# Performance work log

Measured on AMD Instinct MI355X. Metric: run time of the kernel, lower is better.

Reference implementation:

```python
import jax, jax.numpy as jnp
import numpy as np


def kmax_dmp(x, pool_ranges, k_per, K):
    """Vectorized dynamic k-max pooling (order-preserving top-k along time).

    x: [B, T, C] float. pool_ranges: [B] int (per-sample valid prefix length).
    k_per: [B] int (per-sample k, k_per[i] <= pool_ranges[i]). K: static max k.
    Returns [B, K, C]; rows beyond k_per[i] are zero-padded (like pad_sequence).
    """
    B, T, C = x.shape
    neg = jnp.finfo(x.dtype).min
    valid = jnp.arange(T)[None, :] < pool_ranges[:, None]            # [B,T]
    xm = jnp.where(valid[:, :, None], x, neg)
    vals, idx = jax.lax.top_k(jnp.swapaxes(xm, 1, 2), K)             # [B,C,K]
    keep = jnp.arange(K)[None, None, :] < k_per[:, None, None]       # [B,1,K] bcast
    idx = jnp.where(keep, idx, T)                                    # sentinel for dropped slots
    order = jnp.argsort(idx, axis=-1)                                # restore temporal order
    vals = jnp.take_along_axis(vals, order, axis=-1)
    idx = jnp.take_along_axis(idx, order, axis=-1)
    vals = jnp.where(idx < T, vals, jnp.zeros((), x.dtype))          # zero-pad tail
    return jnp.swapaxes(vals, 1, 2)                                  # [B,K,C]


def setup_inputs() -> dict:
    key = jax.random.key(0)
    ks = jax.random.split(key, 8)
    B, T, C = 64, 512, 300
    x = jax.random.normal(ks[0], (B, T, C), jnp.float32)
    lengths = jnp.sort(jax.random.randint(ks[1], (B,), 16, T + 1))[::-1]
    lengths = lengths.at[0].set(T)  # packed sequences are sorted desc; max len == T
    w1 = jax.random.normal(ks[2], (3 * C, 2, 7), jnp.float32) * 0.05        # groups=C//2 -> 2 in-ch/group
    b1 = jax.random.normal(ks[3], (3 * C,), jnp.float32) * 0.05
    w2 = jax.random.normal(ks[4], (14 * C // 4, 2, 6, 5), jnp.float32) * 0.05  # groups=C//4 -> 2 in-ch/group
    b2 = jax.random.normal(ks[5], (14 * C // 4,), jnp.float32) * 0.05
    wfc = jax.random.normal(ks[6], (1, 4 * 14 * C // 4), jnp.float32) * 0.05
    bfc = jax.random.normal(ks[7], (1,), jnp.float32) * 0.05
    return {"x": x, "lengths": lengths, "w1": w1, "b1": b1,
            "w2": w2, "b2": b2, "wfc": wfc, "bfc": bfc}


def reference(x, lengths, w1, b1, w2, b2, wfc, bfc):
    B, T, C = x.shape
    G1, G2 = C // 2, C // 4
    TOP_K, KS1, KS2W = 4, 7, 5
    # zero out padded tail (pad_packed_sequence semantics)
    mask = (jnp.arange(T)[None, :] < lengths[:, None]).astype(x.dtype)
    x = x * mask[:, :, None]
    # grouped conv1d: [B,C,T] -> [B,3C,T+6]
    h = jax.lax.conv_general_dilated(
        jnp.swapaxes(x, 1, 2), w1, (1,), [(KS1 - 1, KS1 - 1)],
        dimension_numbers=("NCH", "OIH", "NCH"), feature_group_count=G1)
    h = h + b1[None, :, None]
    h = jnp.swapaxes(h, 1, 2)                                       # [B,T+6,3C]
    # layer-1 dynamic k-max: k_i = max(top_k, ceil((2-1)/2 * len_i))
    k1 = jnp.maximum(TOP_K, (lengths + 1) // 2)
    K1 = max(TOP_K, (T + 1) // 2)                                   # static (max len == T)
    h = kmax_dmp(h, lengths + (KS1 - 1), k1, K1)                    # [B,K1,3C]
    h = jnp.tanh(jnp.swapaxes(h, 1, 2).reshape(B, G1, 6, K1))       # [B,C//2,6,K1]
    # grouped conv2d: -> [B,14*C//4,1,K1+4]
    h = jax.lax.conv_general_dilated(
        h, w2, (1, 1), [(0, 0), (KS2W - 1, KS2W - 1)],
        dimension_numbers=("NCHW", "OIHW", "NCHW"), feature_group_count=G2)
    h = h + b2[None, :, None, None]
    Wd = K1 + KS2W - 1
    h = h.reshape(B, G2, 14, Wd).transpose(0, 3, 2, 1)              # [B,Wd,14,C//4]
    h = h.reshape(B, Wd, 14 * G2)
    # layer-2 dynamic k-max: k = top_k = 4; valid prefix = k1 + 4
    h = kmax_dmp(h, k1 + (KS2W - 1), jnp.full((B,), TOP_K, lengths.dtype), TOP_K)
    h = jnp.tanh(h).reshape(B, -1)                                  # [B,4*14*C//4]
    out = h @ wfc.T + bfc                                           # [B,1]
    return jnp.concatenate([jnp.zeros_like(out), out], axis=1)      # [B,2]
```

## Files before the change

### kernel.cpp

```cpp
#include <hip/hip_runtime.h>
#include <cstdint>
#include <cstddef>

#define BB   64
#define TT   512
#define CC   300
#define NG1  150
#define OC1  900
#define L1   518
#define K1   256
#define NG2  75
#define W2LEN 260

__device__ __forceinline__ unsigned f2key(float f) {
    unsigned u = __float_as_uint(f);
    return (u & 0x80000000u) ? ~u : (u | 0x80000000u);
}

__global__ void init_out(const float* __restrict__ bfc, float* __restrict__ out) {
    int i = threadIdx.x;
    if (i < 2 * BB) out[i] = (i & 1) ? bfc[0] : 0.0f;
}

__global__ __launch_bounds__(384) void conv1_kmax(
    const float* __restrict__ x, const int* __restrict__ lengths,
    const float* __restrict__ w1, const float* __restrict__ b1,
    float* __restrict__ y1)
{
    const int g   = blockIdx.x;
    const int b   = blockIdx.y;
    const int tid = threadIdx.x;
    const int len = lengths[b];
    const int n   = len + 6;
    const int k   = max(4, (len + 1) >> 1);

    __shared__ float xs[2][524];
    __shared__ float hrow[6][584];
    __shared__ float ws1[84];
    __shared__ float bs1[6];

    if (tid < 84) ws1[tid] = w1[g * 84 + tid];
    if (tid < 6)  bs1[tid] = b1[g * 6 + tid];

    for (int p = tid; p < 2 * 524; p += 384) {
        int ic = p / 524, q = p - ic * 524;
        int t  = q - 6;
        float v = 0.0f;
        if (t >= 0 && t < len) v = x[((size_t)b * TT + t) * CC + (2 * g + ic)];
        xs[ic][q] = v;
    }
    __syncthreads();

    for (int i = tid; i < 6 * L1; i += 384) {
        int r = i / L1, t = i - r * L1;
        if (t < n) {
            float acc = bs1[r];
            #pragma unroll
            for (int ic = 0; ic < 2; ++ic)
                #pragma unroll
                for (int kk = 0; kk < 7; ++kk)
                    acc = fmaf(xs[ic][t + kk], ws1[r * 14 + ic * 7 + kk], acc);
            hrow[r][t] = acc;
        }
    }
    __syncthreads();

    const int r    = tid >> 6;
    const int lane = tid & 63;

    float    v[9];
    unsigned key[9];
    #pragma unroll
    for (int j = 0; j < 9; ++j) {
        int  t     = lane + 64 * j;
        bool valid = (t < n);
        float vv   = hrow[r][t];
        v[j]   = valid ? vv : 0.0f;
        key[j] = valid ? f2key(vv) : 0u;
    }

    unsigned lo = 1u, hi = 0xFFFFFFFFu;
    while (lo < hi) {
        unsigned mid = lo + ((hi - lo + 1) >> 1);
        int c = 0;
        #pragma unroll
        for (int j = 0; j < 9; ++j) c += (key[j] >= mid) ? 1 : 0;
        for (int o = 32; o; o >>= 1) c += __shfl_xor(c, o);
        if (c >= k) lo = mid; else hi = mid - 1;
    }
    const unsigned tau = lo;

    int cg = 0;
    #pragma unroll
    for (int j = 0; j < 9; ++j) cg += (key[j] > tau) ? 1 : 0;
    for (int o = 32; o; o >>= 1) cg += __shfl_xor(cg, o);
    const int budget = k - cg;

    float* outrow = y1 + ((size_t)(b * OC1 + g * 6 + r)) * K1;
    const unsigned long long below = (1ull << lane) - 1ull;

    int baseG = 0, baseE = 0;
    #pragma unroll
    for (int j = 0; j < 9; ++j) {
        bool isG = key[j] > tau;
        bool isE = (key[j] == tau);
        unsigned long long mG = __ballot(isG);
        unsigned long long mE = __ballot(isE);
        int A = baseG + __popcll(mG & below);
        int E = baseE + __popcll(mE & below);
        if (isG || (isE && E < budget)) {
            int pos = A + (E < budget ? E : budget);
            outrow[pos] = tanhf(v[j]);
        }
        baseG += __popcll(mG);
        baseE += __popcll(mE);
    }
    for (int w = k + lane; w < K1; w += 64) outrow[w] = 0.0f;
}

__global__ __launch_bounds__(256) void conv2_kmax_fc(
    const float* __restrict__ y1, const int* __restrict__ lengths,
    const float* __restrict__ w2, const float* __restrict__ b2,
    const float* __restrict__ wfc, float* __restrict__ out)
{
    const int g   = blockIdx.x;
    const int b   = blockIdx.y;
    const int tid = threadIdx.x;
    const int len = lengths[b];
    const int k1  = max(4, (len + 1) >> 1);
    const int n2  = k1 + 4;

    __shared__ float ys[12][264];
    __shared__ float hs[14][264];
    __shared__ float ws2[14 * 60];
    __shared__ float bs2[14];
    __shared__ float partial[14];

    for (int i = tid; i < 14 * 60; i += 256) ws2[i] = w2[(size_t)g * 840 + i];
    if (tid < 14) bs2[tid] = b2[g * 14 + tid];

    for (int i = tid; i < 12 * 264; i += 256) {
        int c = i / 264, p = i - c * 264;
        int w = p - 4;
        float vv = 0.0f;
        if (w >= 0 && w < K1) vv = y1[((size_t)(b * OC1 + g * 12 + c)) * K1 + w];
        ys[c][p] = vv;
    }
    __syncthreads();

    for (int i = tid; i < 14 * W2LEN; i += 256) {
        int r2 = i / W2LEN, w = i - r2 * W2LEN;
        if (w < n2) {
            float acc = bs2[r2];
            #pragma unroll
            for (int c = 0; c < 12; ++c)
                #pragma unroll
                for (int kw = 0; kw < 5; ++kw)
                    acc = fmaf(ys[c][w + kw], ws2[r2 * 60 + c * 5 + kw], acc);
            hs[r2][w] = acc;
        }
    }
    __syncthreads();

    if (tid < 14) {
        const int r2 = tid;
        float tv0 = -INFINITY, tv1 = -INFINITY, tv2 = -INFINITY, tv3 = -INFINITY;
        int   ti0 = 1 << 30,   ti1 = 1 << 30,   ti2 = 1 << 30,   ti3 = 1 << 30;
        for (int w = 0; w < n2; ++w) {
            float vv = hs[r2][w];
            if (vv > tv3) {
                if (vv > tv0)      { tv3=tv2; ti3=ti2; tv2=tv1; ti2=ti1; tv1=tv0; ti1=ti0; tv0=vv; ti0=w; }
                else if (vv > tv1) { tv3=tv2; ti3=ti2; tv2=tv1; ti2=ti1; tv1=vv; ti1=w; }
                else if (vv > tv2) { tv3=tv2; ti3=ti2; tv2=vv; ti2=w; }
                else               { tv3=vv; ti3=w; }
            }
        }
        #define CSWAP(a,bq) if (ti##a > ti##bq) { int t_=ti##a; ti##a=ti##bq; ti##bq=t_; float f_=tv##a; tv##a=tv##bq; tv##bq=f_; }
        CSWAP(0,1) CSWAP(2,3) CSWAP(0,2) CSWAP(1,3) CSWAP(1,2)
        #undef CSWAP
        const int f = r2 * 75 + g;
        float s = 0.0f;
        s += tanhf(tv0) * wfc[0 * 1050 + f];
        s += tanhf(tv1) * wfc[1 * 1050 + f];
        s += tanhf(tv2) * wfc[2 * 1050 + f];
        s += tanhf(tv3) * wfc[3 * 1050 + f];
        partial[r2] = s;
    }
    __syncthreads();

    if (tid == 0) {
        float s = 0.0f;
        #pragma unroll
        for (int i = 0; i < 14; ++i) s += partial[i];
        atomicAdd(&out[b * 2 + 1], s);
    }
}

extern "C" void kernel_launch(void* const* d_in, const int* in_sizes, int n_in,
                              void* d_out, int out_size, void* d_ws, size_t ws_size,
                              hipStream_t stream) {
    const float* x       = (const float*)d_in[0];
    const int*   lengths = (const int*)  d_in[1];
    const float* w1      = (const float*)d_in[2];
    const float* b1      = (const float*)d_in[3];
    const float* w2      = (const float*)d_in[4];
    const float* b2      = (const float*)d_in[5];
    const float* wfc     = (const float*)d_in[6];
    const float* bfc     = (const float*)d_in[7];
    float* out = (float*)d_out;
    float* y1  = (float*)d_ws;

    init_out<<<dim3(1), dim3(128), 0, stream>>>(bfc, out);
    conv1_kmax<<<dim3(NG1, BB), dim3(384), 0, stream>>>(x, lengths, w1, b1, y1);
    conv2_kmax_fc<<<dim3(NG2, BB), dim3(256), 0, stream>>>(y1, lengths, w2, b2, wfc, out);
}
```

Baseline: 397.7 us.

## Fuse conv into register top-k selection and parallelize layer-2 top-4 via wave argmax

Conv1 now computes each output directly into registers inside the k-max wave instead of staging rows through shared memory, and loops are bounded by the valid length. Its threshold binary search counts with ballot+popcount instead of shuffle reductions. Conv2 computes four outputs per lane with float4 shared loads and finds the top-4 using packed value/index keys and wave-wide shuffle argmax, replacing the single-thread serial scan per row. The changes remove a shared-memory round trip, a barrier and serial selection work, at the cost of higher register pressure and per-wave atomics.

```diff
diff --git a/kernel.cpp b/kernel.cpp
--- a/kernel.cpp
+++ b/kernel.cpp
@@ -15,6 +15,13 @@
 __device__ __forceinline__ unsigned f2key(float f) {
     unsigned u = __float_as_uint(f);
     return (u & 0x80000000u) ? ~u : (u | 0x80000000u);
+}
+__device__ __forceinline__ float key2f(unsigned k) {
+    unsigned u = (k & 0x80000000u) ? (k & 0x7FFFFFFFu) : ~k;
+    return __uint_as_float(u);
+}
+__device__ __forceinline__ unsigned long long packvi(float v, int w) {
+    return ((unsigned long long)f2key(v) << 32) | (unsigned)(~(unsigned)w);
 }
 
 __global__ void init_out(const float* __restrict__ bfc, float* __restrict__ out) {
@@ -33,17 +40,18 @@
     const int len = lengths[b];
     const int n   = len + 6;
     const int k   = max(4, (len + 1) >> 1);
+    const int jmax = (n + 63) >> 6;
 
     __shared__ float xs[2][524];
-    __shared__ float hrow[6][584];
-    __shared__ float ws1[84];
-    __shared__ float bs1[6];
-
-    if (tid < 84) ws1[tid] = w1[g * 84 + tid];
-    if (tid < 6)  bs1[tid] = b1[g * 6 + tid];
+    __shared__ float ws1s[84];
+    __shared__ float bs1s[6];
+
+    if (tid < 84) ws1s[tid] = w1[g * 84 + tid];
+    if (tid < 6)  bs1s[tid] = b1[g * 6 + tid];
 
     for (int p = tid; p < 2 * 524; p += 384) {
-        int ic = p / 524, q = p - ic * 524;
+        int ic = (p >= 524) ? 1 : 0;
+        int q  = p - ic * 524;
         int t  = q - 6;
         float v = 0.0f;
         if (t >= 0 && t < len) v = x[((size_t)b * TT + t) * CC + (2 * g + ic)];
@@ -51,32 +59,32 @@
     }
     __syncthreads();
 
-    for (int i = tid; i < 6 * L1; i += 384) {
-        int r = i / L1, t = i - r * L1;
-        if (t < n) {
-            float acc = bs1[r];
-            #pragma unroll
-            for (int ic = 0; ic < 2; ++ic)
-                #pragma unroll
-                for (int kk = 0; kk < 7; ++kk)
-                    acc = fmaf(xs[ic][t + kk], ws1[r * 14 + ic * 7 + kk], acc);
-            hrow[r][t] = acc;
-        }
-    }
-    __syncthreads();
-
     const int r    = tid >> 6;
     const int lane = tid & 63;
 
+    float wr[14];
+    #pragma unroll
+    for (int i = 0; i < 14; ++i) wr[i] = ws1s[r * 14 + i];
+    const float br = bs1s[r];
+
     float    v[9];
     unsigned key[9];
     #pragma unroll
     for (int j = 0; j < 9; ++j) {
-        int  t     = lane + 64 * j;
-        bool valid = (t < n);
-        float vv   = hrow[r][t];
-        v[j]   = valid ? vv : 0.0f;
-        key[j] = valid ? f2key(vv) : 0u;
+        v[j] = 0.0f; key[j] = 0u;
+        if (j < jmax) {
+            int t = lane + 64 * j;
+            if (t < n) {
+                float acc = br;
+                #pragma unroll
+                for (int ic = 0; ic < 2; ++ic)
+                    #pragma unroll
+                    for (int kk = 0; kk < 7; ++kk)
+                        acc = fmaf(xs[ic][t + kk], wr[ic * 7 + kk], acc);
+                v[j]   = acc;
+                key[j] = f2key(acc);
+            }
+        }
     }
 
     unsigned lo = 1u, hi = 0xFFFFFFFFu;
@@ -84,16 +92,16 @@
         unsigned mid = lo + ((hi - lo + 1) >> 1);
         int c = 0;
         #pragma unroll
-        for (int j = 0; j < 9; ++j) c += (key[j] >= mid) ? 1 : 0;
-        for (int o = 32; o; o >>= 1) c += __shfl_xor(c, o);
+        for (int j = 0; j < 9; ++j)
+            if (j < jmax) c += (int)__popcll(__ballot(key[j] >= mid));
         if (c >= k) lo = mid; else hi = mid - 1;
     }
     const unsigned tau = lo;
 
     int cg = 0;
     #pragma unroll
-    for (int j = 0; j < 9; ++j) cg += (key[j] > tau) ? 1 : 0;
-    for (int o = 32; o; o >>= 1) cg += __shfl_xor(cg, o);
+    for (int j = 0; j < 9; ++j)
+        if (j < jmax) cg += (int)__popcll(__ballot(key[j] > tau));
     const int budget = k - cg;
 
     float* outrow = y1 + ((size_t)(b * OC1 + g * 6 + r)) * K1;
@@ -102,18 +110,20 @@
     int baseG = 0, baseE = 0;
     #pragma unroll
     for (int j = 0; j < 9; ++j) {
-        bool isG = key[j] > tau;
-        bool isE = (key[j] == tau);
-        unsigned long long mG = __ballot(isG);
-        unsigned long long mE = __ballot(isE);
-        int A = baseG + __popcll(mG & below);
-        int E = baseE + __popcll(mE & below);
-        if (isG || (isE && E < budget)) {
-            int pos = A + (E < budget ? E : budget);
-            outrow[pos] = tanhf(v[j]);
-        }
-        baseG += __popcll(mG);
-        baseE += __popcll(mE);
+        if (j < jmax) {
+            bool isG = key[j] > tau;
+            bool isE = (key[j] == tau);
+            unsigned long long mG = __ballot(isG);
+            unsigned long long mE = __ballot(isE);
+            int A = baseG + (int)__popcll(mG & below);
+            int E = baseE + (int)__popcll(mE & below);
+            if (isG || (isE && E < budget)) {
+                int pos = A + (E < budget ? E : budget);
+                outrow[pos] = tanhf(v[j]);
+            }
+            baseG += (int)__popcll(mG);
+            baseE += (int)__popcll(mE);
+        }
     }
     for (int w = k + lane; w < K1; w += 64) outrow[w] = 0.0f;
 }
@@ -130,14 +140,12 @@
     const int k1  = max(4, (len + 1) >> 1);
     const int n2  = k1 + 4;
 
-    __shared__ float ys[12][264];
-    __shared__ float hs[14][264];
-    __shared__ float ws2[14 * 60];
-    __shared__ float bs2[14];
-    __shared__ float partial[14];
-
-    for (int i = tid; i < 14 * 60; i += 256) ws2[i] = w2[(size_t)g * 840 + i];
-    if (tid < 14) bs2[tid] = b2[g * 14 + tid];
+    __shared__ __align__(16) float ys[12][264];
+    __shared__ float ws2s[840];
+    __shared__ float bs2s[14];
+
+    for (int i = tid; i < 840; i += 256) ws2s[i] = w2[(size_t)g * 840 + i];
+    if (tid < 14) bs2s[tid] = b2[g * 14 + tid];
 
     for (int i = tid; i < 12 * 264; i += 256) {
         int c = i / 264, p = i - c * 264;
@@ -148,52 +156,85 @@
     }
     __syncthreads();
 
-    for (int i = tid; i < 14 * W2LEN; i += 256) {
-        int r2 = i / W2LEN, w = i - r2 * W2LEN;
-        if (w < n2) {
-            float acc = bs2[r2];
+    const int wv   = tid >> 6;
+    const int lane = tid & 63;
+    float wsum = 0.0f;
+
+    for (int r2 = wv; r2 < 14; r2 += 4) {
+        const float bias = bs2s[r2];
+        float acc0 = bias, acc1 = bias, acc2 = bias, acc3 = bias;
+
+        #pragma unroll 4
+        for (int c = 0; c < 12; ++c) {
+            const float4 f0 = *(const float4*)&ys[c][4 * lane];
+            const float4 f1 = *(const float4*)&ys[c][4 * lane + 4];
+            const float e0=f0.x,e1=f0.y,e2=f0.z,e3=f0.w,e4=f1.x,e5=f1.y,e6=f1.z,e7=f1.w;
+            const float q0 = ws2s[r2*60 + c*5 + 0];
+            const float q1 = ws2s[r2*60 + c*5 + 1];
+            const float q2 = ws2s[r2*60 + c*5 + 2];
+            const float q3 = ws2s[r2*60 + c*5 + 3];
+            const float q4 = ws2s[r2*60 + c*5 + 4];
+            acc0=fmaf(e0,q0,acc0); acc0=fmaf(e1,q1,acc0); acc0=fmaf(e2,q2,acc0); acc0=fmaf(e3,q3,acc0); acc0=fmaf(e4,q4,acc0);
+            acc1=fmaf(e1,q0,acc1); acc1=fmaf(e2,q1,acc1); acc1=fmaf(e3,q2,acc1); acc1=fmaf(e4,q3,acc1); acc1=fmaf(e5,q4,acc1);
+            acc2=fmaf(e2,q0,acc2); acc2=fmaf(e3,q1,acc2); acc2=fmaf(e4,q2,acc2); acc2=fmaf(e5,q3,acc2); acc2=fmaf(e6,q4,acc2);
+            acc3=fmaf(e3,q0,acc3); acc3=fmaf(e4,q1,acc3); acc3=fmaf(e5,q2,acc3); acc3=fmaf(e6,q3,acc3); acc3=fmaf(e7,q4,acc3);
+        }
+
+        const int w0i = 4 * lane;
+        unsigned long long cand0 = (w0i + 0 < n2) ? packvi(acc0, w0i + 0) : 0ull;
+        unsigned long long cand1 = (w0i + 1 < n2) ? packvi(acc1, w0i + 1) : 0ull;
+        unsigned long long cand2 = (w0i + 2 < n2) ? packvi(acc2, w0i + 2) : 0ull;
+        unsigned long long cand3 = (w0i + 3 < n2) ? packvi(acc3, w0i + 3) : 0ull;
+        unsigned long long cand4 = 0ull;
+        if (n2 > 256) {
+            if (lane < 4) {
+                int w = 256 + lane;
+                float a = bias;
+                #pragma unroll
+                for (int c = 0; c < 12; ++c)
+                    #pragma unroll
+                    for (int kw = 0; kw < 5; ++kw)
+                        a = fmaf(ys[c][w + kw], ws2s[r2*60 + c*5 + kw], a);
+                if (w < n2) cand4 = packvi(a, w);
+            }
+        }
+
+        float tv[4]; int ti[4];
+        #pragma unroll
+        for (int round = 0; round < 4; ++round) {
+            unsigned long long best = cand0;
+            best = cand1 > best ? cand1 : best;
+            best = cand2 > best ? cand2 : best;
+            best = cand3 > best ? cand3 : best;
+            best = cand4 > best ? cand4 : best;
             #pragma unroll
-            for (int c = 0; c < 12; ++c)
-                #pragma unroll
-                for (int kw = 0; kw < 5; ++kw)
-                    acc = fmaf(ys[c][w + kw], ws2[r2 * 60 + c * 5 + kw], acc);
-            hs[r2][w] = acc;
-        }
-    }
-    __syncthreads();
-
-    if (tid < 14) {
-        const int r2 = tid;
-        float tv0 = -INFINITY, tv1 = -INFINITY, tv2 = -INFINITY, tv3 = -INFINITY;
-        int   ti0 = 1 << 30,   ti1 = 1 << 30,   ti2 = 1 << 30,   ti3 = 1 << 30;
-        for (int w = 0; w < n2; ++w) {
-            float vv = hs[r2][w];
-            if (vv > tv3) {
-                if (vv > tv0)      { tv3=tv2; ti3=ti2; tv2=tv1; ti2=ti1; tv1=tv0; ti1=ti0; tv0=vv; ti0=w; }
-                else if (vv > tv1) { tv3=tv2; ti3=ti2; tv2=tv1; ti2=ti1; tv1=vv; ti1=w; }
-                else if (vv > tv2) { tv3=tv2; ti3=ti2; tv2=vv; ti2=w; }
-                else               { tv3=vv; ti3=w; }
-            }
-        }
-        #define CSWAP(a,bq) if (ti##a > ti##bq) { int t_=ti##a; ti##a=ti##bq; ti##bq=t_; float f_=tv##a; tv##a=tv##bq; tv##bq=f_; }
-        CSWAP(0,1) CSWAP(2,3) CSWAP(0,2) CSWAP(1,3) CSWAP(1,2)
-        #undef CSWAP
+            for (int o = 32; o; o >>= 1) {
+                unsigned bh = (unsigned)(best >> 32), bl = (unsigned)best;
+                unsigned oh = __shfl_xor(bh, o),      ol = __shfl_xor(bl, o);
+                unsigned long long other = ((unsigned long long)oh << 32) | ol;
+                if (other > best) best = other;
+            }
+            ti[round] = (int)(~(unsigned)best);
+            tv[round] = key2f((unsigned)(best >> 32));
+            if (cand0 == best) cand0 = 0ull;
+            if (cand1 == best) cand1 = 0ull;
+            if (cand2 == best) cand2 = 0ull;
+            if (cand3 == best) cand3 = 0ull;
+            if (cand4 == best) cand4 = 0ull;
+        }
+        #define CSW(a,bq) if (ti[a] > ti[bq]) { int t_=ti[a]; ti[a]=ti[bq]; ti[bq]=t_; float f_=tv[a]; tv[a]=tv[bq]; tv[bq]=f_; }
+        CSW(0,1) CSW(2,3) CSW(0,2) CSW(1,3) CSW(1,2)
+        #undef CSW
+
         const int f = r2 * 75 + g;
-        float s = 0.0f;
-        s += tanhf(tv0) * wfc[0 * 1050 + f];
-        s += tanhf(tv1) * wfc[1 * 1050 + f];
-        s += tanhf(tv2) * wfc[2 * 1050 + f];
-        s += tanhf(tv3) * wfc[3 * 1050 + f];
-        partial[r2] = s;
-    }
-    __syncthreads();
-
-    if (tid == 0) {
-        float s = 0.0f;
-        #pragma unroll
-        for (int i = 0; i < 14; ++i) s += partial[i];
-        atomicAdd(&out[b * 2 + 1], s);
-    }
+        float s = tanhf(tv[0]) * wfc[0 * 1050 + f];
+        s = fmaf(tanhf(tv[1]), wfc[1 * 1050 + f], s);
+        s = fmaf(tanhf(tv[2]), wfc[2 * 1050 + f], s);
+        s = fmaf(tanhf(tv[3]), wfc[3 * 1050 + f], s);
+        wsum += s;
+    }
+
+    if (lane == 0) atomicAdd(&out[b * 2 + 1], wsum);
 }
 
 extern "C" void kernel_launch(void* const* d_in, const int* in_sizes, int n_in,
```

After: 396.2 us. Within noise of the previous version (-0.4%).
